# Kernel optimization log

Measured on AMD Instinct MI355X. Metric: run time of the kernel, lower is better.

## Reference

```python
import jax, jax.numpy as jnp
import numpy as np

N = 100000; E = 1600000; G = 2000; S = 40; MAXP = 50
IN = 64; F = 128; H = 4; HD = F // H; FFN = 8 * F
EPS = 1e-5; BN_EPS = 1e-5

def _ln(x, g, b):
    m = jnp.mean(x, -1, keepdims=True)
    v = jnp.mean((x - m) ** 2, -1, keepdims=True)
    return (x - m) * jax.lax.rsqrt(v + EPS) * g + b

def setup_inputs():
    key = jax.random.key(0)
    ks = jax.random.split(key, 16)
    def lin(k, i, o):
        kw, kb = jax.random.split(k)
        lim = 1.0 / np.sqrt(i)
        return (jax.random.uniform(kw, (i, o), jnp.float32, -lim, lim),
                jax.random.uniform(kb, (o,), jnp.float32, -lim, lim))
    W_gcn, b_gcn = lin(ks[1], IN, F)
    Wq, bq = lin(ks[2], F, F); Wk, bk = lin(ks[3], F, F)
    Wv, bv = lin(ks[4], F, F); Wo, bo = lin(ks[5], F, F)
    W1, b1 = lin(ks[6], F, FFN); W2, b2 = lin(ks[7], FFN, F)
    Wg, bg = lin(ks[8], 2 * F, F)
    ones = lambda: jnp.ones((F,), jnp.float32)
    zeros = lambda: jnp.zeros((F,), jnp.float32)
    return {
        'x': jax.random.normal(ks[0], (N, IN), jnp.float32),
        'edge_index': jax.random.randint(ks[9], (2, E), 0, N),
        'batch': jnp.repeat(jnp.arange(G), N // G),
        'set_batch': jnp.repeat(jnp.arange(S), G // S),
        'W_gcn': W_gcn, 'b_gcn': b_gcn,
        'bn_g': ones(), 'bn_b': zeros(),
        'lnpre_g': ones(), 'lnpre_b': zeros(),
        'Wq': Wq, 'bq': bq, 'Wk': Wk, 'bk': bk, 'Wv': Wv, 'bv': bv, 'Wo': Wo, 'bo': bo,
        'ln1_g': ones(), 'ln1_b': zeros(),
        'W1': W1, 'b1': b1, 'W2': W2, 'b2': b2,
        'ln2_g': ones(), 'ln2_b': zeros(),
        'Wg': Wg, 'bg': bg,
    }

def _forward(x, W_gcn, b_gcn, bn_g, bn_b, lnpre_g, lnpre_b, Wq, bq, Wk, bk, Wv, bv, Wo, bo, ln1_g, ln1_b, W1, b1, W2, b2, ln2_g, ln2_b, Wg, bg, edge_index, batch, set_batch):
    row, col = edge_index[0], edge_index[1]
    # GCNConv, improved=True -> self-loop weight 2.0 (PyG gcn_norm)
    xw = x @ W_gcn                                              # [N,F]
    deg = jax.ops.segment_sum(jnp.ones(E, xw.dtype), col, N) + 2.0
    dinv = jax.lax.rsqrt(deg)
    norm = dinv[row] * dinv[col]                                # [E]
    agg = jax.ops.segment_sum(xw[row] * norm[:, None], col, N)  # scatter-add to targets
    h = agg + (2.0 * dinv * dinv)[:, None] * xw + b_gcn
    # BatchNorm1d eval (running_mean=0, running_var=1) + ReLU; dropout is identity in eval
    h = jax.nn.relu(h * jax.lax.rsqrt(jnp.asarray(1.0 + BN_EPS, h.dtype)) * bn_g + bn_b)
    # global mean pool per graph
    cnt_g = jax.ops.segment_sum(jnp.ones(N, h.dtype), batch, G)
    z = jax.ops.segment_sum(h, batch, G) / cnt_g[:, None]       # [G,F]
    # to_dense_batch over sets (set_batch is sorted)
    cnt_s = jax.ops.segment_sum(jnp.ones(G, jnp.int32), set_batch, S)
    starts = jnp.cumsum(cnt_s) - cnt_s
    pos = jnp.arange(G) - starts[set_batch]                     # position within set
    zd = jnp.zeros((S, MAXP, F), z.dtype).at[set_batch, pos].set(z)
    mask = jnp.arange(MAXP)[None, :] < cnt_s[:, None]           # [S,MAXP]
    # pre-LN MHA with key_padding_mask
    zn = _ln(zd, lnpre_g, lnpre_b)
    q = (zn @ Wq + bq).reshape(S, MAXP, H, HD)
    k = (zn @ Wk + bk).reshape(S, MAXP, H, HD)
    v = (zn @ Wv + bv).reshape(S, MAXP, H, HD)
    scores = jnp.einsum('sqhd,skhd->shqk', q, k) / np.sqrt(HD)
    scores = jnp.where(mask[:, None, None, :], scores, -1e9)
    attn = jax.nn.softmax(scores, -1)
    o = jnp.einsum('shqk,skhd->sqhd', attn, v).reshape(S, MAXP, F) @ Wo + bo
    zd = _ln(zd + o, ln1_g, ln1_b)
    # FFN block (post-LN residual)
    f = jax.nn.relu(zd @ W1 + b1) @ W2 + b2
    zd = _ln(zd + f, ln2_g, ln2_b)
    # z_dense[mask] ordering == gather via (set_batch, pos); broadcast to nodes
    set_info = zd[set_batch, pos][batch]                        # [N,F]
    # gated fusion
    gate = jax.nn.sigmoid(jnp.concatenate([h, set_info], -1) @ Wg + bg)
    return gate * set_info + (1.0 - gate) * h

def reference(x, edge_index, batch, set_batch, W_gcn, b_gcn, bn_g, bn_b, lnpre_g, lnpre_b, Wq, bq, Wk, bk, Wv, bv, Wo, bo, ln1_g, ln1_b, W1, b1, W2, b2, ln2_g, ln2_b, Wg, bg):
    return _forward(x, W_gcn, b_gcn, bn_g, bn_b, lnpre_g, lnpre_b, Wq, bq, Wk, bk, Wv, bv, Wo, bo, ln1_g, ln1_b, W1, b1, W2, b2, ln2_g, ln2_b, Wg, bg, edge_index, batch, set_batch)
```

## Files before the change

kernel.cpp:

```cpp
#include <hip/hip_runtime.h>
#include <hip/hip_bf16.h>
#include <cstddef>

#define NN 100000
#define NE 1600000
#define NG 2000
#define NS 40
#define INF 64
#define F 128
#define FFN_DIM 1024
#define NB 782
#define BCAP 3072
#define SC_BLOCKS 512
#define SC_CHUNK 3125
#define NXB 782
#define NWB 72

using bf16 = __hip_bfloat16;
typedef __attribute__((ext_vector_type(8))) short short8;
typedef __attribute__((ext_vector_type(4))) float f32x4;
typedef __attribute__((ext_vector_type(2))) float f32x2;

__device__ __forceinline__ short f2bs(float f){
    union { bf16 b; short s; } u; u.b = __float2bfloat16(f); return u.s;
}
__device__ __forceinline__ unsigned int pk2(float a, float b){
    return (unsigned int)(unsigned short)f2bs(a) | ((unsigned int)(unsigned short)f2bs(b) << 16);
}

__global__ __launch_bounds__(256) void k_xws(const float* __restrict__ x, const float* __restrict__ W,
                                             const float* __restrict__ dinv, unsigned char* __restrict__ xws8,
                                             const float* __restrict__ Wq, const float* __restrict__ Wk,
                                             const float* __restrict__ Wv, const float* __restrict__ Wo,
                                             const float* __restrict__ W1, const float* __restrict__ W2,
                                             const float* __restrict__ Wg,
                                             unsigned short* __restrict__ Wqb, unsigned short* __restrict__ Wkb,
                                             unsigned short* __restrict__ Wvb, unsigned short* __restrict__ Wob,
                                             unsigned short* __restrict__ W1b, unsigned short* __restrict__ W2b,
                                             unsigned short* __restrict__ Wgb, unsigned short* __restrict__ Wgbotb){
    int t = threadIdx.x;
    if (blockIdx.x >= NXB){
        int wt = (blockIdx.x - NXB)*256 + t;
        const int ws = NWB*256;
        for (int i=wt; i<16384; i+=ws){
            int k = i>>7, n = i&127;
            Wqb[n*128+k]    = (unsigned short)f2bs(Wq[(size_t)k*F+n]);
            Wkb[n*128+k]    = (unsigned short)f2bs(Wk[(size_t)k*F+n]);
            Wvb[n*128+k]    = (unsigned short)f2bs(Wv[(size_t)k*F+n]);
            Wob[n*128+k]    = (unsigned short)f2bs(Wo[(size_t)k*F+n]);
            Wgb[n*128+k]    = (unsigned short)f2bs(Wg[(size_t)k*F+n]);
            Wgbotb[n*128+k] = (unsigned short)f2bs(Wg[(size_t)(F+k)*F+n]);
        }
        for (int i=wt; i<131072; i+=ws){
            int k = i>>10, n = i&1023;
            W1b[(size_t)n*128+k] = (unsigned short)f2bs(W1[(size_t)k*FFN_DIM+n]);
        }
        for (int i=wt; i<131072; i+=ws){
            int n = i>>10, k = i&1023;
            W2b[(size_t)n*1024+k] = (unsigned short)f2bs(W2[(size_t)k*F+n]);
        }
        return;
    }
    __shared__ short Xs[128*72];
    __shared__ short Ws[128*72];
    int rowBase = blockIdx.x * 128;
    #pragma unroll
    for (int i=0;i<32;i++){
        int id = i*256+t; int k = id>>7, n = id&127;
        Ws[n*72 + k] = f2bs(W[id]);
    }
    #pragma unroll
    for (int i=0;i<8;i++){
        int id = i*256+t;
        int r = id>>4; int k4 = (id&15)*4;
        int row = rowBase + r; if (row >= NN) row = NN-1;
        float4 v = *(const float4*)&x[(size_t)row*INF + k4];
        *(unsigned int*)&Xs[r*72 + k4]     = pk2(v.x, v.y);
        *(unsigned int*)&Xs[r*72 + k4 + 2] = pk2(v.z, v.w);
    }
    __syncthreads();
    int lane = t & 63, w = t >> 6;
    int lr = lane & 15, quad = lane >> 4;
    f32x4 acc[2][8];
    #pragma unroll
    for (int i=0;i<2;i++)
        #pragma unroll
        for (int j=0;j<8;j++) acc[i][j] = (f32x4){0.f,0.f,0.f,0.f};
    #pragma unroll
    for (int ks=0; ks<2; ++ks){
        int kb = ks*32 + quad*8;
        short8 b0 = *(const short8*)&Xs[((w  )*16 + lr)*72 + kb];
        short8 b1 = *(const short8*)&Xs[((w+4)*16 + lr)*72 + kb];
        #pragma unroll
        for (int mt=0; mt<8; ++mt){
            short8 a = *(const short8*)&Ws[(mt*16 + lr)*72 + kb];
            acc[0][mt] = __builtin_amdgcn_mfma_f32_16x16x32_bf16(a, b0, acc[0][mt], 0, 0, 0);
            acc[1][mt] = __builtin_amdgcn_mfma_f32_16x16x32_bf16(a, b1, acc[1][mt], 0, 0, 0);
        }
    }
    #pragma unroll
    for (int rt=0; rt<2; ++rt){
        int row = rowBase + (w + rt*4)*16 + lr;
        if (row < NN){
            float dv = dinv[row];
            #pragma unroll
            for (int mt=0; mt<8; ++mt){
                int p = __builtin_amdgcn_cvt_pk_fp8_f32(acc[rt][mt][0]*dv, acc[rt][mt][1]*dv, 0, false);
                p     = __builtin_amdgcn_cvt_pk_fp8_f32(acc[rt][mt][2]*dv, acc[rt][mt][3]*dv, p, true);
                *(int*)&xws8[(size_t)row*F + mt*16 + quad*4] = p;
            }
        }
    }
}

__global__ __launch_bounds__(1024) void k_scatter2(const int* __restrict__ ei, int* __restrict__ bcursor,
                                                   int* __restrict__ ebuf){
    __shared__ int lh[NB];
    __shared__ int lb[NB];
    int t = threadIdx.x;
    int base = blockIdx.x * SC_CHUNK;
    for (int b=t; b<NB; b+=1024) lh[b] = 0;
    __syncthreads();
    int rr[4], cc[4];
    #pragma unroll
    for (int q=0;q<4;q++){
        int i = t + q*1024;
        bool v = (i < SC_CHUNK);
        int idx = v ? (base + i) : base;
        rr[q] = ei[idx];
        cc[q] = ei[NE + idx];
        if (v) atomicAdd(&lh[cc[q]>>7], 1);
    }
    __syncthreads();
    for (int b=t; b<NB; b+=1024){
        int n = lh[b];
        lb[b] = n ? (b*BCAP + atomicAdd(&bcursor[b], n)) : 0;
        lh[b] = 0;
    }
    __syncthreads();
    #pragma unroll
    for (int q=0;q<4;q++){
        int i = t + q*1024;
        if (i < SC_CHUNK){
            int b = cc[q] >> 7;
            int rk = atomicAdd(&lh[b], 1);
            ebuf[lb[b] + rk] = (rr[q] << 7) | (cc[q] & 127);
        }
    }
}

__global__ __launch_bounds__(256) void k_sort(const int* __restrict__ ebuf, const int* __restrict__ bcursor,
                                              int* __restrict__ cnt, float* __restrict__ dinv,
                                              int* __restrict__ nstart, int* __restrict__ ebuf2){
    __shared__ int lh[128];
    __shared__ int s[128];
    __shared__ int lcur[128];
    __shared__ int sorted[BCAP];
    int t = threadIdx.x;
    int b = blockIdx.x;
    int e0 = b * BCAP;
    int nE = bcursor[b];
    if (t < 128) lh[t] = 0;
    __syncthreads();
    for (int i=t; i<nE; i+=256) atomicAdd(&lh[ebuf[e0+i] & 127], 1);
    __syncthreads();
    int c = (t < 128) ? lh[t] : 0;
    if (t < 128) s[t] = c;
    __syncthreads();
    #pragma unroll
    for (int off=1; off<128; off<<=1){
        int v = (t >= off && t < 128) ? s[t-off] : 0;
        __syncthreads();
        if (t < 128) s[t] += v;
        __syncthreads();
    }
    int node = b*128 + t;
    if (t < 128){
        int excl = s[t] - c;
        lcur[t] = excl;
        if (node < NN){
            nstart[node] = e0 + excl;
            cnt[node] = c;
            dinv[node] = rsqrtf((float)c + 2.0f);
        }
    }
    __syncthreads();
    for (int i=t; i<nE; i+=256){
        int v = ebuf[e0 + i];
        int nl = v & 127;
        int rk = atomicAdd(&lcur[nl], 1);
        sorted[rk] = (v >> 7) << 5;
    }
    __syncthreads();
    for (int i=t; i<nE; i+=256) ebuf2[e0 + i] = sorted[i];
}

__global__ __launch_bounds__(256) void k_aggpool(const unsigned char* __restrict__ xws8,
                                                 const int* __restrict__ nstart, const int* __restrict__ cnt,
                                                 const float* __restrict__ dinv, const float* __restrict__ b_gcn,
                                                 const float* __restrict__ bn_g, const float* __restrict__ bn_b,
                                                 const int* __restrict__ ebuf2,
                                                 const float* __restrict__ lnpre_g, const float* __restrict__ lnpre_b,
                                                 float* __restrict__ h, unsigned short* __restrict__ hb,
                                                 float* __restrict__ z, unsigned short* __restrict__ znb){
    __shared__ float zacc[4][128];
    int t = threadIdx.x;
    int lane = t & 63, w = t >> 6;
    int half = lane >> 5, lh = lane & 31;
    int g = blockIdx.x;
    const unsigned int* xw32 = (const unsigned int*)xws8;
    unsigned int* hb32 = (unsigned int*)hb;
    unsigned int* znb32 = (unsigned int*)znb;

    float4 bg4  = *(const float4*)&b_gcn[4*lh];
    float4 bng4 = *(const float4*)&bn_g[4*lh];
    float4 bnb4 = *(const float4*)&bn_b[4*lh];
    const float bns = rsqrtf(1.f + 1e-5f);

    float za0=0.f, za1=0.f, za2=0.f, za3=0.f;

    for (int i = w; i < 50; i += 4){
        int node = g*50 + i;
        int s0n = nstart[node]; int dg = cnt[node]; float dv = dinv[node];
        unsigned int us = xw32[node*32 + lh];
        float a0=0.f, a1=0.f, a2=0.f, a3=0.f;
        int j=0;
        for (; j+8<=dg; j+=8){
            int r0 = ebuf2[s0n+j+0+half];
            int r1 = ebuf2[s0n+j+2+half];
            int r2 = ebuf2[s0n+j+4+half];
            int r3 = ebuf2[s0n+j+6+half];
            unsigned int u0 = xw32[r0 + lh];
            unsigned int u1 = xw32[r1 + lh];
            unsigned int u2 = xw32[r2 + lh];
            unsigned int u3 = xw32[r3 + lh];
            f32x2 l0 = __builtin_amdgcn_cvt_pk_f32_fp8(u0, false);
            f32x2 h0 = __builtin_amdgcn_cvt_pk_f32_fp8(u0, true);
            f32x2 l1 = __builtin_amdgcn_cvt_pk_f32_fp8(u1, false);
            f32x2 h1 = __builtin_amdgcn_cvt_pk_f32_fp8(u1, true);
            f32x2 l2 = __builtin_amdgcn_cvt_pk_f32_fp8(u2, false);
            f32x2 h2 = __builtin_amdgcn_cvt_pk_f32_fp8(u2, true);
            f32x2 l3 = __builtin_amdgcn_cvt_pk_f32_fp8(u3, false);
            f32x2 h3 = __builtin_amdgcn_cvt_pk_f32_fp8(u3, true);
            a0 += (l0.x + l1.x) + (l2.x + l3.x);
            a1 += (l0.y + l1.y) + (l2.y + l3.y);
            a2 += (h0.x + h1.x) + (h2.x + h3.x);
            a3 += (h0.y + h1.y) + (h2.y + h3.y);
        }
        for (; j+2<=dg; j+=2){
            int r0 = ebuf2[s0n+j+half];
            unsigned int u0 = xw32[r0 + lh];
            f32x2 l0 = __builtin_amdgcn_cvt_pk_f32_fp8(u0, false);
            f32x2 h0 = __builtin_amdgcn_cvt_pk_f32_fp8(u0, true);
            a0 += l0.x; a1 += l0.y; a2 += h0.x; a3 += h0.y;
        }
        if (j < dg && half == 0){
            int r0 = ebuf2[s0n+j];
            unsigned int u0 = xw32[r0 + lh];
            f32x2 l0 = __builtin_amdgcn_cvt_pk_f32_fp8(u0, false);
            f32x2 h0 = __builtin_amdgcn_cvt_pk_f32_fp8(u0, true);
            a0 += l0.x; a1 += l0.y; a2 += h0.x; a3 += h0.y;
        }
        a0 += __shfl_xor(a0, 32);
        a1 += __shfl_xor(a1, 32);
        a2 += __shfl_xor(a2, 32);
        a3 += __shfl_xor(a3, 32);
        f32x2 fl = __builtin_amdgcn_cvt_pk_f32_fp8(us, false);
        f32x2 fh = __builtin_amdgcn_cvt_pk_f32_fp8(us, true);
        float p0 = dv*(a0 + 2.f*fl.x) + bg4.x;
        float p1 = dv*(a1 + 2.f*fl.y) + bg4.y;
        float p2 = dv*(a2 + 2.f*fh.x) + bg4.z;
        float p3 = dv*(a3 + 2.f*fh.y) + bg4.w;
        p0 = fmaxf(p0*bns*bng4.x + bnb4.x, 0.f);
        p1 = fmaxf(p1*bns*bng4.y + bnb4.y, 0.f);
        p2 = fmaxf(p2*bns*bng4.z + bnb4.z, 0.f);
        p3 = fmaxf(p3*bns*bng4.w + bnb4.w, 0.f);
        if (half == 0){
            *(float4*)&h[(size_t)node*F + 4*lh] = make_float4(p0,p1,p2,p3);
            *(uint2*)&hb32[(size_t)node*64 + 2*lh] = make_uint2(pk2(p0,p1), pk2(p2,p3));
        }
        za0 += p0; za1 += p1; za2 += p2; za3 += p3;
    }
    if (half == 0)
        *(float4*)&zacc[w][4*lh] = make_float4(za0, za1, za2, za3);
    __syncthreads();
    if (w == 0){
        float4 v0 = *(const float4*)&zacc[0][4*lh];
        float4 v1 = *(const float4*)&zacc[1][4*lh];
        float4 v2 = *(const float4*)&zacc[2][4*lh];
        float4 v3 = *(const float4*)&zacc[3][4*lh];
        float s0 = ((v0.x+v1.x)+(v2.x+v3.x)) / 50.0f;
        float s1 = ((v0.y+v1.y)+(v2.y+v3.y)) / 50.0f;
        float s2 = ((v0.z+v1.z)+(v2.z+v3.z)) / 50.0f;
        float s3 = ((v0.w+v1.w)+(v2.w+v3.w)) / 50.0f;
        if (half == 0)
            *(float4*)&z[(size_t)g*F + 4*lh] = make_float4(s0,s1,s2,s3);
        float s = (s0+s1)+(s2+s3);
        #pragma unroll
        for (int off=1; off<32; off<<=1) s += __shfl_xor(s, off);
        float m = s * (1.f/128.f);
        float d0=s0-m, d1=s1-m, d2=s2-m, d3=s3-m;
        float vv = (d0*d0+d1*d1)+(d2*d2+d3*d3);
        #pragma unroll
        for (int off=1; off<32; off<<=1) vv += __shfl_xor(vv, off);
        float rs = rsqrtf(vv*(1.f/128.f) + 1e-5f);
        float4 lg = *(const float4*)&lnpre_g[4*lh];
        float4 lb = *(const float4*)&lnpre_b[4*lh];
        if (half == 0){
            float o0 = d0*rs*lg.x+lb.x, o1 = d1*rs*lg.y+lb.y;
            float o2 = d2*rs*lg.z+lb.z, o3 = d3*rs*lg.w+lb.w;
            *(uint2*)&znb32[(size_t)g*64 + 2*lh] = make_uint2(pk2(o0,o1), pk2(o2,o3));
        }
    }
}

__global__ __launch_bounds__(256) void k_settf2(const unsigned short* __restrict__ znb,
                                                const float* __restrict__ z,
                                                const unsigned short* __restrict__ Wqb,
                                                const unsigned short* __restrict__ Wkb,
                                                const unsigned short* __restrict__ Wvb,
                                                const float* __restrict__ bq, const float* __restrict__ bk,
                                                const float* __restrict__ bv,
                                                const unsigned short* __restrict__ Wob, const float* __restrict__ bo,
                                                const float* __restrict__ ln1_g, const float* __restrict__ ln1_b,
                                                const unsigned short* __restrict__ W1b, const float* __restrict__ b1,
                                                const unsigned short* __restrict__ W2b, const float* __restrict__ b2,
                                                const float* __restrict__ ln2_g, const float* __restrict__ ln2_b,
                                                const unsigned short* __restrict__ Wgbotb, const float* __restrict__ bg,
                                                float* __restrict__ zd2, float* __restrict__ gsi){
    __shared__ __align__(16) char smem[138208];
    float* Sc   = (float*)smem;
    float* qs   = (float*)(smem + 41600);
    float* ks   = (float*)(smem + 68000);
    float* vs   = (float*)(smem + 94400);
    short* aob  = (short*)(smem + 120800);
    float* zd1f = (float*)(smem + 41600);
    short* zd1b = (short*)(smem + 68000);
    short* f1b  = (short*)(smem + 94400);
    short* zd2b = f1b;

    int t = threadIdx.x;
    int lane = t & 63, w = t >> 6;
    int lr = lane & 15, quad = lane >> 4;
    int s = blockIdx.x;
    const int r0 = s*50;

    {
        int rl = w*16 + lr; if (rl > 49) rl = 49;
        const unsigned short* arow = &znb[(size_t)(r0 + rl)*F];
        for (int zsel=0; zsel<3; ++zsel){
            const unsigned short* B = (zsel==0)?Wqb:(zsel==1)?Wkb:Wvb;
            const float* bp = (zsel==0)?bq:(zsel==1)?bk:bv;
            float* outp = (zsel==0)?qs:(zsel==1)?ks:vs;
            f32x4 acc[8];
            #pragma unroll
            for (int j=0;j<8;j++) acc[j] = (f32x4){0.f,0.f,0.f,0.f};
            #pragma unroll
            for (int ks4=0; ks4<4; ++ks4){
                int kb = ks4*32 + quad*8;
                short8 a = *(const short8*)&arow[kb];
                #pragma unroll
                for (int nt=0; nt<8; ++nt){
                    short8 b = *(const short8*)&B[(size_t)(nt*16 + lr)*128 + kb];
                    acc[nt] = __builtin_amdgcn_mfma_f32_16x16x32_bf16(a, b, acc[nt], 0, 0, 0);
                }
            }
            #pragma unroll
            for (int r=0; r<4; ++r){
                int row = w*16 + quad*4 + r;
                if (row < 50){
                    #pragma unroll
                    for (int nt=0; nt<8; ++nt){
                        int col = nt*16 + lr;
                        outp[row*132 + col] = acc[nt][r] + bp[col];
                    }
                }
            }
        }
    }
    __syncthreads();

    {
        int hh = w;
        float* ScH = Sc + hh*50*52;
        int qi = lane;
        if (qi < 50){
            float qreg[32];
            #pragma unroll
            for (int d=0; d<32; ++d) qreg[d] = qs[qi*132 + hh*32 + d];
            for (int ki=0; ki<50; ++ki){
                float acc=0.f;
                #pragma unroll
                for (int d=0; d<32; ++d) acc += qreg[d] * ks[ki*132 + hh*32 + d];
                ScH[qi*52 + ki] = acc * 0.17677669529663687f;
            }
            float m=-1e30f;
            for (int ki=0; ki<50; ++ki) m = fmaxf(m, ScH[qi*52+ki]);
            float sum=0.f;
            for (int ki=0; ki<50; ++ki){ float e=__expf(ScH[qi*52+ki]-m); ScH[qi*52+ki]=e; sum+=e; }
            float inv = 1.f/sum;
            float o[32];
            #pragma unroll
            for (int d=0; d<32; ++d) o[d] = 0.f;
            for (int ki=0; ki<50; ++ki){
                float sc = ScH[qi*52+ki] * inv;
                #pragma unroll
                for (int d=0; d<32; ++d) o[d] += sc * vs[ki*132 + hh*32 + d];
            }
            #pragma unroll
            for (int d=0; d<32; ++d) aob[qi*136 + hh*32 + d] = f2bs(o[d]);
        } else if (qi < 64){
            #pragma unroll
            for (int d=0; d<32; ++d) aob[qi*136 + hh*32 + d] = 0;
        }
    }
    __syncthreads();

    {
        f32x4 acc[8];
        #pragma unroll
        for (int j=0;j<8;j++) acc[j] = (f32x4){0.f,0.f,0.f,0.f};
        #pragma unroll
        for (int ks4=0; ks4<4; ++ks4){
            int kb = ks4*32 + quad*8;
            short8 a = *(const short8*)&aob[(w*16 + lr)*136 + kb];
            #pragma unroll
            for (int nt=0; nt<8; ++nt){
                short8 b = *(const short8*)&Wob[(size_t)(nt*16 + lr)*128 + kb];
                acc[nt] = __builtin_amdgcn_mfma_f32_16x16x32_bf16(a, b, acc[nt], 0, 0, 0);
            }
        }
        #pragma unroll
        for (int r=0; r<4; ++r){
            int row = w*16 + quad*4 + r;
            float v[8];
            if (row < 50){
                #pragma unroll
                for (int nt=0; nt<8; ++nt){
                    int col = nt*16 + lr;
                    v[nt] = acc[nt][r] + bo[col] + z[(size_t)(r0+row)*F + col];
                }
            } else {
                #pragma unroll
                for (int nt=0; nt<8; ++nt) v[nt] = 0.f;
            }
            float ssum = 0.f;
            #pragma unroll
            for (int nt=0; nt<8; ++nt) ssum += v[nt];
            #pragma unroll
            for (int off=1; off<16; off<<=1) ssum += __shfl_xor(ssum, off);
            float mean = ssum * (1.f/128.f);
            float var = 0.f;
            float d[8];
            #pragma unroll
            for (int nt=0; nt<8; ++nt){ d[nt] = v[nt]-mean; var += d[nt]*d[nt]; }
            #pragma unroll
            for (int off=1; off<16; off<<=1) var += __shfl_xor(var, off);
            float rsv = rsqrtf(var*(1.f/128.f) + 1e-5f);
            if (row < 50){
                #pragma unroll
                for (int nt=0; nt<8; ++nt){
                    int col = nt*16 + lr;
                    float o = d[nt]*rsv*ln1_g[col] + ln1_b[col];
                    zd1f[row*132 + col] = o;
                    zd1b[row*136 + col] = f2bs(o);
                }
            } else {
                #pragma unroll
                for (int nt=0; nt<8; ++nt) zd1b[row*136 + nt*16 + lr] = 0;
            }
        }
    }
    __syncthreads();

    f32x4 acc2[8];
    #pragma unroll
    for (int j=0;j<8;j++) acc2[j] = (f32x4){0.f,0.f,0.f,0.f};
    for (int c=0; c<8; ++c){
        f32x4 a1[8];
        #pragma unroll
        for (int j=0;j<8;j++) a1[j] = (f32x4){0.f,0.f,0.f,0.f};
        #pragma unroll
        for (int ks4=0; ks4<4; ++ks4){
            int kb = ks4*32 + quad*8;
            short8 a = *(const short8*)&zd1b[(w*16 + lr)*136 + kb];
            #pragma unroll
            for (int nt=0; nt<8; ++nt){
                short8 b = *(const short8*)&W1b[(size_t)(c*128 + nt*16 + lr)*128 + kb];
                a1[nt] = __builtin_amdgcn_mfma_f32_16x16x32_bf16(a, b, a1[nt], 0, 0, 0);
            }
        }
        #pragma unroll
        for (int r=0; r<4; ++r){
            int row = w*16 + quad*4 + r;
            #pragma unroll
            for (int nt=0; nt<8; ++nt){
                int col = nt*16 + lr;
                f1b[row*136 + col] = f2bs(fmaxf(a1[nt][r] + b1[c*128 + col], 0.f));
            }
        }
        __syncthreads();
        #pragma unroll
        for (int ks4=0; ks4<4; ++ks4){
            int kb = ks4*32 + quad*8;
            short8 a = *(const short8*)&f1b[(w*16 + lr)*136 + kb];
            #pragma unroll
            for (int nt=0; nt<8; ++nt){
                short8 b = *(const short8*)&W2b[(size_t)(nt*16 + lr)*1024 + c*128 + kb];
                acc2[nt] = __builtin_amdgcn_mfma_f32_16x16x32_bf16(a, b, acc2[nt], 0, 0, 0);
            }
        }
        __syncthreads();
    }

    {
        #pragma unroll
        for (int r=0; r<4; ++r){
            int row = w*16 + quad*4 + r;
            float v[8];
            if (row < 50){
                #pragma unroll
                for (int nt=0; nt<8; ++nt){
                    int col = nt*16 + lr;
                    v[nt] = acc2[nt][r] + b2[col] + zd1f[row*132 + col];
                }
            } else {
                #pragma unroll
                for (int nt=0; nt<8; ++nt) v[nt] = 0.f;
            }
            float ssum = 0.f;
            #pragma unroll
            for (int nt=0; nt<8; ++nt) ssum += v[nt];
            #pragma unroll
            for (int off=1; off<16; off<<=1) ssum += __shfl_xor(ssum, off);
            float mean = ssum * (1.f/128.f);
            float var = 0.f;
            float d[8];
            #pragma unroll
            for (int nt=0; nt<8; ++nt){ d[nt] = v[nt]-mean; var += d[nt]*d[nt]; }
            #pragma unroll
            for (int off=1; off<16; off<<=1) var += __shfl_xor(var, off);
            float rsv = rsqrtf(var*(1.f/128.f) + 1e-5f);
            if (row < 50){
                #pragma unroll
                for (int nt=0; nt<8; ++nt){
                    int col = nt*16 + lr;
                    float o = d[nt]*rsv*ln2_g[col] + ln2_b[col];
                    zd2[(size_t)(r0+row)*F + col] = o;
                    zd2b[row*136 + col] = f2bs(o);
                }
            } else {
                #pragma unroll
                for (int nt=0; nt<8; ++nt) zd2b[row*136 + nt*16 + lr] = 0;
            }
        }
        __syncthreads();
        f32x4 ag[8];
        #pragma unroll
        for (int j=0;j<8;j++) ag[j] = (f32x4){0.f,0.f,0.f,0.f};
        #pragma unroll
        for (int ks4=0; ks4<4; ++ks4){
            int kb = ks4*32 + quad*8;
            short8 a = *(const short8*)&zd2b[(w*16 + lr)*136 + kb];
            #pragma unroll
            for (int nt=0; nt<8; ++nt){
                short8 b = *(const short8*)&Wgbotb[(size_t)(nt*16 + lr)*128 + kb];
                ag[nt] = __builtin_amdgcn_mfma_f32_16x16x32_bf16(a, b, ag[nt], 0, 0, 0);
            }
        }
        #pragma unroll
        for (int r=0; r<4; ++r){
            int row = w*16 + quad*4 + r;
            if (row < 50){
                #pragma unroll
                for (int nt=0; nt<8; ++nt){
                    int col = nt*16 + lr;
                    gsi[(size_t)(r0+row)*F + col] = ag[nt][r] + bg[col];
                }
            }
        }
    }
}

__global__ __launch_bounds__(256) void k_gate_mfma(const float* __restrict__ h,
                                                   const unsigned short* __restrict__ hb,
                                                   const unsigned short* __restrict__ Wgb,
                                                   const float* __restrict__ gsi, const float* __restrict__ zd2,
                                                   float* __restrict__ out){
    int t = threadIdx.x;
    int lane = t & 63, w = t >> 6;
    int lr = lane & 15, quad = lane >> 4;
    int mrow0 = blockIdx.x*64 + w*16;
    f32x4 acc[8];
    #pragma unroll
    for (int j=0;j<8;j++) acc[j] = (f32x4){0.f,0.f,0.f,0.f};
    #pragma unroll
    for (int ks=0; ks<4; ++ks){
        int kb = ks*32 + quad*8;
        int row = mrow0 + lr;
        if (row >= NN) row = NN-1;
        short8 a = *(const short8*)&hb[(size_t)row*F + kb];
        #pragma unroll
        for (int nt=0; nt<8; ++nt){
            short8 b = *(const short8*)&Wgb[(size_t)(nt*16 + lr)*128 + kb];
            acc[nt] = __builtin_amdgcn_mfma_f32_16x16x32_bf16(a, b, acc[nt], 0, 0, 0);
        }
    }
    #pragma unroll
    for (int r=0; r<4; ++r){
        int row = mrow0 + quad*4 + r;
        if (row >= NN) continue;
        int g = row / 50;
        const float* gs = &gsi[(size_t)g*F];
        const float* zs = &zd2[(size_t)g*F];
        const float* hr = &h[(size_t)row*F];
        float* orow = &out[(size_t)row*F];
        #pragma unroll
        for (int nt=0; nt<8; ++nt){
            int col = nt*16 + lr;
            float L = acc[nt][r] + gs[col];
            float gate = 1.f/(1.f + __expf(-L));
            orow[col] = gate*zs[col] + (1.f-gate)*hr[col];
        }
    }
}

extern "C" void kernel_launch(void* const* d_in, const int* in_sizes, int n_in,
                              void* d_out, int out_size, void* d_ws, size_t ws_size,
                              hipStream_t stream) {
    const float* x      = (const float*)d_in[0];
    const int*   ei     = (const int*)d_in[1];
    const float* W_gcn  = (const float*)d_in[4];
    const float* b_gcn  = (const float*)d_in[5];
    const float* bn_g   = (const float*)d_in[6];
    const float* bn_b   = (const float*)d_in[7];
    const float* lnpre_g= (const float*)d_in[8];
    const float* lnpre_b= (const float*)d_in[9];
    const float* Wq     = (const float*)d_in[10];
    const float* bq     = (const float*)d_in[11];
    const float* Wk     = (const float*)d_in[12];
    const float* bk     = (const float*)d_in[13];
    const float* Wv     = (const float*)d_in[14];
    const float* bv     = (const float*)d_in[15];
    const float* Wo     = (const float*)d_in[16];
    const float* bo     = (const float*)d_in[17];
    const float* ln1_g  = (const float*)d_in[18];
    const float* ln1_b  = (const float*)d_in[19];
    const float* W1     = (const float*)d_in[20];
    const float* b1     = (const float*)d_in[21];
    const float* W2     = (const float*)d_in[22];
    const float* b2     = (const float*)d_in[23];
    const float* ln2_g  = (const float*)d_in[24];
    const float* ln2_b  = (const float*)d_in[25];
    const float* Wg     = (const float*)d_in[26];
    const float* bg     = (const float*)d_in[27];
    float* out = (float*)d_out;
    char* ws = (char*)d_ws;

    size_t o = 0;
    unsigned char* xws8 = (unsigned char*)(ws + o); o += (size_t)NN*F;
    float* h     = (float*)(ws + o); o += (size_t)NN*F*4;
    unsigned short* hb = (unsigned short*)(ws + o); o += (size_t)NN*F*2;
    int*   cnt   = (int*)(ws + o);   o += (size_t)NN*4;
    int*   nstart= (int*)(ws + o);   o += (size_t)NN*4;
    int*   ebuf  = (int*)(ws + o);   o += (size_t)NB*BCAP*4;
    int*   ebuf2 = (int*)(ws + o);   o += (size_t)NB*BCAP*4;
    float* dinv  = (float*)(ws + o); o += (size_t)NN*4;
    int*   bcursor=(int*)(ws + o);   o += 1024*4;
    unsigned short* Wgb    = (unsigned short*)(ws + o); o += 16384*2;
    unsigned short* Wqb    = (unsigned short*)(ws + o); o += 16384*2;
    unsigned short* Wkb    = (unsigned short*)(ws + o); o += 16384*2;
    unsigned short* Wvb    = (unsigned short*)(ws + o); o += 16384*2;
    unsigned short* Wob    = (unsigned short*)(ws + o); o += 16384*2;
    unsigned short* Wgbotb = (unsigned short*)(ws + o); o += 16384*2;
    unsigned short* W1b = (unsigned short*)(ws + o); o += (size_t)131072*2;
    unsigned short* W2b = (unsigned short*)(ws + o); o += (size_t)131072*2;
    float* z     = (float*)(ws + o); o += (size_t)NG*F*4;
    unsigned short* znb = (unsigned short*)(ws + o); o += (size_t)NG*F*2;
    float* zd2   = (float*)(ws + o); o += (size_t)NG*F*4;
    float* gsi   = (float*)(ws + o); o += (size_t)NG*F*4;

    hipMemsetAsync(bcursor, 0, (size_t)NB*4, stream);
    k_scatter2<<<SC_BLOCKS, 1024, 0, stream>>>(ei, bcursor, ebuf);
    k_sort<<<NB, 256, 0, stream>>>(ebuf, bcursor, cnt, dinv, nstart, ebuf2);
    k_xws<<<NXB + NWB, 256, 0, stream>>>(x, W_gcn, dinv, xws8,
                                         Wq, Wk, Wv, Wo, W1, W2, Wg,
                                         Wqb, Wkb, Wvb, Wob, W1b, W2b, Wgb, Wgbotb);
    k_aggpool<<<NG, 256, 0, stream>>>(xws8, nstart, cnt, dinv, b_gcn, bn_g, bn_b, ebuf2,
                                      lnpre_g, lnpre_b, h, hb, z, znb);

    k_settf2<<<NS, 256, 0, stream>>>(znb, z, Wqb, Wkb, Wvb, bq, bk, bv,
                                     Wob, bo, ln1_g, ln1_b, W1b, b1, W2b, b2,
                                     ln2_g, ln2_b, Wgbotb, bg, zd2, gsi);

    k_gate_mfma<<<(NN+63)/64, 256, 0, stream>>>(h, hb, Wgb, gsi, zd2, out);
}
```

Baseline: 373.4 us.

## Split set transformer into QKV-in-pool, per-head attention, and row-tiled post kernels

Replaces the single set-transformer kernel, which ran on only 40 blocks, with three stages. The Q/K/V projections are folded into the pooling kernel as per-graph fp32 matvecs, attention runs in a separate kernel with one block per set and head (160 blocks), and the Wo/LN/FFN/LN/gate projection runs in a 16-row-tiled MFMA kernel over 125 blocks. The aim is to remove the low-parallelism serial tail. In exchange it adds two kernel launches and global round trips for q/k/v/attention output, and the QKV projection now uses fp32 scalar math with uncached weight reads.

```diff
diff --git a/kernel.cpp b/kernel.cpp
--- a/kernel.cpp
+++ b/kernel.cpp
@@ -30,23 +30,17 @@
 
 __global__ __launch_bounds__(256) void k_xws(const float* __restrict__ x, const float* __restrict__ W,
                                              const float* __restrict__ dinv, unsigned char* __restrict__ xws8,
-                                             const float* __restrict__ Wq, const float* __restrict__ Wk,
-                                             const float* __restrict__ Wv, const float* __restrict__ Wo,
-                                             const float* __restrict__ W1, const float* __restrict__ W2,
-                                             const float* __restrict__ Wg,
-                                             unsigned short* __restrict__ Wqb, unsigned short* __restrict__ Wkb,
-                                             unsigned short* __restrict__ Wvb, unsigned short* __restrict__ Wob,
-                                             unsigned short* __restrict__ W1b, unsigned short* __restrict__ W2b,
-                                             unsigned short* __restrict__ Wgb, unsigned short* __restrict__ Wgbotb){
+                                             const float* __restrict__ Wo, const float* __restrict__ W1,
+                                             const float* __restrict__ W2, const float* __restrict__ Wg,
+                                             unsigned short* __restrict__ Wob, unsigned short* __restrict__ W1b,
+                                             unsigned short* __restrict__ W2b, unsigned short* __restrict__ Wgb,
+                                             unsigned short* __restrict__ Wgbotb){
     int t = threadIdx.x;
     if (blockIdx.x >= NXB){
         int wt = (blockIdx.x - NXB)*256 + t;
         const int ws = NWB*256;
         for (int i=wt; i<16384; i+=ws){
             int k = i>>7, n = i&127;
-            Wqb[n*128+k]    = (unsigned short)f2bs(Wq[(size_t)k*F+n]);
-            Wkb[n*128+k]    = (unsigned short)f2bs(Wk[(size_t)k*F+n]);
-            Wvb[n*128+k]    = (unsigned short)f2bs(Wv[(size_t)k*F+n]);
             Wob[n*128+k]    = (unsigned short)f2bs(Wo[(size_t)k*F+n]);
             Wgb[n*128+k]    = (unsigned short)f2bs(Wg[(size_t)k*F+n]);
             Wgbotb[n*128+k] = (unsigned short)f2bs(Wg[(size_t)(F+k)*F+n]);
@@ -201,8 +195,13 @@
                                                  const float* __restrict__ bn_g, const float* __restrict__ bn_b,
                                                  const int* __restrict__ ebuf2,
                                                  const float* __restrict__ lnpre_g, const float* __restrict__ lnpre_b,
+                                                 const float* __restrict__ Wq, const float* __restrict__ bq,
+                                                 const float* __restrict__ Wk, const float* __restrict__ bk,
+                                                 const float* __restrict__ Wv, const float* __restrict__ bv,
                                                  float* __restrict__ h, unsigned short* __restrict__ hb,
-                                                 float* __restrict__ z, unsigned short* __restrict__ znb){
+                                                 float* __restrict__ z,
+                                                 float* __restrict__ qb, float* __restrict__ kb2,
+                                                 float* __restrict__ vb){
     __shared__ float zacc[4][128];
     int t = threadIdx.x;
     int lane = t & 63, w = t >> 6;
@@ -210,7 +209,6 @@
     int g = blockIdx.x;
     const unsigned int* xw32 = (const unsigned int*)xws8;
     unsigned int* hb32 = (unsigned int*)hb;
-    unsigned int* znb32 = (unsigned int*)znb;
 
     float4 bg4  = *(const float4*)&b_gcn[4*lh];
     float4 bng4 = *(const float4*)&bn_g[4*lh];
@@ -307,276 +305,235 @@
         float4 lg = *(const float4*)&lnpre_g[4*lh];
         float4 lb = *(const float4*)&lnpre_b[4*lh];
         if (half == 0){
-            float o0 = d0*rs*lg.x+lb.x, o1 = d1*rs*lg.y+lb.y;
-            float o2 = d2*rs*lg.z+lb.z, o3 = d3*rs*lg.w+lb.w;
-            *(uint2*)&znb32[(size_t)g*64 + 2*lh] = make_uint2(pk2(o0,o1), pk2(o2,o3));
-        }
-    }
-}
-
-__global__ __launch_bounds__(256) void k_settf2(const unsigned short* __restrict__ znb,
-                                                const float* __restrict__ z,
-                                                const unsigned short* __restrict__ Wqb,
-                                                const unsigned short* __restrict__ Wkb,
-                                                const unsigned short* __restrict__ Wvb,
-                                                const float* __restrict__ bq, const float* __restrict__ bk,
-                                                const float* __restrict__ bv,
-                                                const unsigned short* __restrict__ Wob, const float* __restrict__ bo,
-                                                const float* __restrict__ ln1_g, const float* __restrict__ ln1_b,
-                                                const unsigned short* __restrict__ W1b, const float* __restrict__ b1,
-                                                const unsigned short* __restrict__ W2b, const float* __restrict__ b2,
-                                                const float* __restrict__ ln2_g, const float* __restrict__ ln2_b,
-                                                const unsigned short* __restrict__ Wgbotb, const float* __restrict__ bg,
-                                                float* __restrict__ zd2, float* __restrict__ gsi){
-    __shared__ __align__(16) char smem[138208];
-    float* Sc   = (float*)smem;
-    float* qs   = (float*)(smem + 41600);
-    float* ks   = (float*)(smem + 68000);
-    float* vs   = (float*)(smem + 94400);
-    short* aob  = (short*)(smem + 120800);
-    float* zd1f = (float*)(smem + 41600);
-    short* zd1b = (short*)(smem + 68000);
-    short* f1b  = (short*)(smem + 94400);
-    short* zd2b = f1b;
-
+            zacc[0][4*lh]   = d0*rs*lg.x+lb.x;
+            zacc[0][4*lh+1] = d1*rs*lg.y+lb.y;
+            zacc[0][4*lh+2] = d2*rs*lg.z+lb.z;
+            zacc[0][4*lh+3] = d3*rs*lg.w+lb.w;
+        }
+    }
+    __syncthreads();
+    for (int idx = t; idx < 384; idx += 256){
+        int sel = idx >> 7, col = idx & 127;
+        const float* Wp = (sel==0) ? Wq : (sel==1) ? Wk : Wv;
+        const float* bi = (sel==0) ? bq : (sel==1) ? bk : bv;
+        float* C = (sel==0) ? qb : (sel==1) ? kb2 : vb;
+        float acc = bi[col];
+        #pragma unroll 4
+        for (int k=0; k<128; ++k) acc += zacc[0][k] * Wp[(size_t)k*F + col];
+        C[(size_t)g*F + col] = acc;
+    }
+}
+
+__global__ __launch_bounds__(256) void k_attn(const float* __restrict__ q, const float* __restrict__ k,
+                                              const float* __restrict__ v, unsigned short* __restrict__ aob){
+    __shared__ float Qs[1600], Ks[1600], Vs[1600], Sc[2500];
+    int t = threadIdx.x;
+    int s = blockIdx.x >> 2; int hh = blockIdx.x & 3;
+    for (int idx=t; idx<1600; idx+=256){
+        int i = idx>>5, d = idx&31;
+        size_t gi = (size_t)(s*50+i)*F + hh*32 + d;
+        Qs[idx]=q[gi]; Ks[idx]=k[gi]; Vs[idx]=v[gi];
+    }
+    __syncthreads();
+    for (int idx=t; idx<2500; idx+=256){
+        int qi = idx/50, ki = idx%50;
+        float acc=0.f;
+        #pragma unroll 8
+        for (int d=0;d<32;d++) acc += Qs[qi*32+d]*Ks[ki*32+d];
+        Sc[idx] = acc * 0.17677669529663687f;
+    }
+    __syncthreads();
+    if (t < 50){
+        float m=-1e30f;
+        for (int j=0;j<50;j++) m = fmaxf(m, Sc[t*50+j]);
+        float sum=0.f;
+        for (int j=0;j<50;j++){ float e=__expf(Sc[t*50+j]-m); Sc[t*50+j]=e; sum+=e; }
+        float inv = 1.f/sum;
+        for (int j=0;j<50;j++) Sc[t*50+j] *= inv;
+    }
+    __syncthreads();
+    for (int idx=t; idx<1600; idx+=256){
+        int qi = idx>>5, d = idx&31;
+        float acc=0.f;
+        #pragma unroll 10
+        for (int ki=0;ki<50;ki++) acc += Sc[qi*50+ki]*Vs[ki*32+d];
+        aob[(size_t)(s*50+qi)*F + hh*32 + d] = (unsigned short)f2bs(acc);
+    }
+}
+
+__global__ __launch_bounds__(256) void k_post(const unsigned short* __restrict__ aob,
+                                              const float* __restrict__ z,
+                                              const unsigned short* __restrict__ Wob, const float* __restrict__ bo,
+                                              const float* __restrict__ ln1_g, const float* __restrict__ ln1_b,
+                                              const unsigned short* __restrict__ W1b, const float* __restrict__ b1,
+                                              const unsigned short* __restrict__ W2b, const float* __restrict__ b2,
+                                              const float* __restrict__ ln2_g, const float* __restrict__ ln2_b,
+                                              const unsigned short* __restrict__ Wgbotb, const float* __restrict__ bg,
+                                              float* __restrict__ zd2, float* __restrict__ gsi){
+    __shared__ float zd1f[16*132];
+    __shared__ short zd1b[16*136];
+    __shared__ short f1b[16*1040];
+    __shared__ short zd2b[16*136];
     int t = threadIdx.x;
     int lane = t & 63, w = t >> 6;
     int lr = lane & 15, quad = lane >> 4;
-    int s = blockIdx.x;
-    const int r0 = s*50;
+    int gr0 = blockIdx.x * 16;
 
     {
-        int rl = w*16 + lr; if (rl > 49) rl = 49;
-        const unsigned short* arow = &znb[(size_t)(r0 + rl)*F];
-        for (int zsel=0; zsel<3; ++zsel){
-            const unsigned short* B = (zsel==0)?Wqb:(zsel==1)?Wkb:Wvb;
-            const float* bp = (zsel==0)?bq:(zsel==1)?bk:bv;
-            float* outp = (zsel==0)?qs:(zsel==1)?ks:vs;
-            f32x4 acc[8];
+        f32x4 accA[2];
+        accA[0] = (f32x4){0.f,0.f,0.f,0.f};
+        accA[1] = (f32x4){0.f,0.f,0.f,0.f};
+        #pragma unroll
+        for (int ks4=0; ks4<4; ++ks4){
+            int kb = ks4*32 + quad*8;
+            short8 a = *(const short8*)&aob[(size_t)(gr0 + lr)*F + kb];
             #pragma unroll
-            for (int j=0;j<8;j++) acc[j] = (f32x4){0.f,0.f,0.f,0.f};
+            for (int j=0;j<2;j++){
+                int nt = 2*w + j;
+                short8 b = *(const short8*)&Wob[(size_t)(nt*16 + lr)*128 + kb];
+                accA[j] = __builtin_amdgcn_mfma_f32_16x16x32_bf16(a, b, accA[j], 0, 0, 0);
+            }
+        }
+        #pragma unroll
+        for (int j=0;j<2;j++){
+            int nt = 2*w + j;
+            #pragma unroll
+            for (int r=0;r<4;r++){
+                int row = quad*4 + r;
+                int col = nt*16 + lr;
+                zd1f[row*132 + col] = accA[j][r] + bo[col] + z[(size_t)(gr0+row)*F + col];
+            }
+        }
+    }
+    __syncthreads();
+    {
+        int tr = t >> 4, l16 = t & 15;
+        float v[8];
+        #pragma unroll
+        for (int i=0;i<8;i++) v[i] = zd1f[tr*132 + l16*8 + i];
+        float s = 0.f;
+        #pragma unroll
+        for (int i=0;i<8;i++) s += v[i];
+        #pragma unroll
+        for (int off=1; off<16; off<<=1) s += __shfl_xor(s, off);
+        float mean = s * (1.f/128.f);
+        float var = 0.f;
+        float d[8];
+        #pragma unroll
+        for (int i=0;i<8;i++){ d[i] = v[i]-mean; var += d[i]*d[i]; }
+        #pragma unroll
+        for (int off=1; off<16; off<<=1) var += __shfl_xor(var, off);
+        float rsv = rsqrtf(var*(1.f/128.f) + 1e-5f);
+        #pragma unroll
+        for (int i=0;i<8;i++){
+            int c = l16*8 + i;
+            float o = d[i]*rsv*ln1_g[c] + ln1_b[c];
+            zd1f[tr*132 + c] = o;
+            zd1b[tr*136 + c] = f2bs(o);
+        }
+    }
+    __syncthreads();
+
+    {
+        short8 a[4];
+        #pragma unroll
+        for (int ks4=0; ks4<4; ++ks4){
+            int kb = ks4*32 + quad*8;
+            a[ks4] = *(const short8*)&zd1b[lr*136 + kb];
+        }
+        for (int nt2=0; nt2<16; ++nt2){
+            int coln = w*256 + nt2*16 + lr;
+            f32x4 acc = (f32x4){0.f,0.f,0.f,0.f};
             #pragma unroll
             for (int ks4=0; ks4<4; ++ks4){
                 int kb = ks4*32 + quad*8;
-                short8 a = *(const short8*)&arow[kb];
-                #pragma unroll
-                for (int nt=0; nt<8; ++nt){
-                    short8 b = *(const short8*)&B[(size_t)(nt*16 + lr)*128 + kb];
-                    acc[nt] = __builtin_amdgcn_mfma_f32_16x16x32_bf16(a, b, acc[nt], 0, 0, 0);
-                }
+                short8 b = *(const short8*)&W1b[(size_t)coln*128 + kb];
+                acc = __builtin_amdgcn_mfma_f32_16x16x32_bf16(a[ks4], b, acc, 0, 0, 0);
             }
             #pragma unroll
-            for (int r=0; r<4; ++r){
-                int row = w*16 + quad*4 + r;
-                if (row < 50){
-                    #pragma unroll
-                    for (int nt=0; nt<8; ++nt){
-                        int col = nt*16 + lr;
-                        outp[row*132 + col] = acc[nt][r] + bp[col];
-                    }
-                }
+            for (int r=0;r<4;r++){
+                int row = quad*4 + r;
+                int col = w*256 + nt2*16 + lr;
+                f1b[row*1040 + col] = f2bs(fmaxf(acc[r] + b1[col], 0.f));
             }
         }
     }
     __syncthreads();
 
+    f32x4 accC[2];
+    accC[0] = (f32x4){0.f,0.f,0.f,0.f};
+    accC[1] = (f32x4){0.f,0.f,0.f,0.f};
+    for (int ks4=0; ks4<32; ++ks4){
+        int kb = ks4*32 + quad*8;
+        short8 a = *(const short8*)&f1b[lr*1040 + kb];
+        #pragma unroll
+        for (int j=0;j<2;j++){
+            int nt = 2*w + j;
+            short8 b = *(const short8*)&W2b[(size_t)(nt*16 + lr)*1024 + kb];
+            accC[j] = __builtin_amdgcn_mfma_f32_16x16x32_bf16(a, b, accC[j], 0, 0, 0);
+        }
+    }
+    #pragma unroll
+    for (int j=0;j<2;j++){
+        int nt = 2*w + j;
+        #pragma unroll
+        for (int r=0;r<4;r++){
+            int row = quad*4 + r;
+            int col = nt*16 + lr;
+            zd1f[row*132 + col] = accC[j][r] + b2[col] + zd1f[row*132 + col];
+        }
+    }
+    __syncthreads();
     {
-        int hh = w;
-        float* ScH = Sc + hh*50*52;
-        int qi = lane;
-        if (qi < 50){
-            float qreg[32];
-            #pragma unroll
-            for (int d=0; d<32; ++d) qreg[d] = qs[qi*132 + hh*32 + d];
-            for (int ki=0; ki<50; ++ki){
-                float acc=0.f;
-                #pragma unroll
-                for (int d=0; d<32; ++d) acc += qreg[d] * ks[ki*132 + hh*32 + d];
-                ScH[qi*52 + ki] = acc * 0.17677669529663687f;
-            }
-            float m=-1e30f;
-            for (int ki=0; ki<50; ++ki) m = fmaxf(m, ScH[qi*52+ki]);
-            float sum=0.f;
-            for (int ki=0; ki<50; ++ki){ float e=__expf(ScH[qi*52+ki]-m); ScH[qi*52+ki]=e; sum+=e; }
-            float inv = 1.f/sum;
-            float o[32];
-            #pragma unroll
-            for (int d=0; d<32; ++d) o[d] = 0.f;
-            for (int ki=0; ki<50; ++ki){
-                float sc = ScH[qi*52+ki] * inv;
-                #pragma unroll
-                for (int d=0; d<32; ++d) o[d] += sc * vs[ki*132 + hh*32 + d];
-            }
-            #pragma unroll
-            for (int d=0; d<32; ++d) aob[qi*136 + hh*32 + d] = f2bs(o[d]);
-        } else if (qi < 64){
-            #pragma unroll
-            for (int d=0; d<32; ++d) aob[qi*136 + hh*32 + d] = 0;
-        }
-    }
-    __syncthreads();
-
+        int tr = t >> 4, l16 = t & 15;
+        float v[8];
+        #pragma unroll
+        for (int i=0;i<8;i++) v[i] = zd1f[tr*132 + l16*8 + i];
+        float s = 0.f;
+        #pragma unroll
+        for (int i=0;i<8;i++) s += v[i];
+        #pragma unroll
+        for (int off=1; off<16; off<<=1) s += __shfl_xor(s, off);
+        float mean = s * (1.f/128.f);
+        float var = 0.f;
+        float d[8];
+        #pragma unroll
+        for (int i=0;i<8;i++){ d[i] = v[i]-mean; var += d[i]*d[i]; }
+        #pragma unroll
+        for (int off=1; off<16; off<<=1) var += __shfl_xor(var, off);
+        float rsv = rsqrtf(var*(1.f/128.f) + 1e-5f);
+        #pragma unroll
+        for (int i=0;i<8;i++){
+            int c = l16*8 + i;
+            float o = d[i]*rsv*ln2_g[c] + ln2_b[c];
+            zd2[(size_t)(gr0+tr)*F + c] = o;
+            zd2b[tr*136 + c] = f2bs(o);
+        }
+    }
+    __syncthreads();
     {
-        f32x4 acc[8];
-        #pragma unroll
-        for (int j=0;j<8;j++) acc[j] = (f32x4){0.f,0.f,0.f,0.f};
+        f32x4 accG[2];
+        accG[0] = (f32x4){0.f,0.f,0.f,0.f};
+        accG[1] = (f32x4){0.f,0.f,0.f,0.f};
         #pragma unroll
         for (int ks4=0; ks4<4; ++ks4){
             int kb = ks4*32 + quad*8;
-            short8 a = *(const short8*)&aob[(w*16 + lr)*136 + kb];
+            short8 a = *(const short8*)&zd2b[lr*136 + kb];
             #pragma unroll
-            for (int nt=0; nt<8; ++nt){
-                short8 b = *(const short8*)&Wob[(size_t)(nt*16 + lr)*128 + kb];
-                acc[nt] = __builtin_amdgcn_mfma_f32_16x16x32_bf16(a, b, acc[nt], 0, 0, 0);
+            for (int j=0;j<2;j++){
+                int nt = 2*w + j;
+                short8 b = *(const short8*)&Wgbotb[(size_t)(nt*16 + lr)*128 + kb];
+                accG[j] = __builtin_amdgcn_mfma_f32_16x16x32_bf16(a, b, accG[j], 0, 0, 0);
             }
         }
         #pragma unroll
-        for (int r=0; r<4; ++r){
-            int row = w*16 + quad*4 + r;
-            float v[8];
-            if (row < 50){
-                #pragma unroll
-                for (int nt=0; nt<8; ++nt){
-                    int col = nt*16 + lr;
-                    v[nt] = acc[nt][r] + bo[col] + z[(size_t)(r0+row)*F + col];
-                }
-            } else {
-                #pragma unroll
-                for (int nt=0; nt<8; ++nt) v[nt] = 0.f;
-            }
-            float ssum = 0.f;
+        for (int j=0;j<2;j++){
+            int nt = 2*w + j;
             #pragma unroll
-            for (int nt=0; nt<8; ++nt) ssum += v[nt];
-            #pragma unroll
-            for (int off=1; off<16; off<<=1) ssum += __shfl_xor(ssum, off);
-            float mean = ssum * (1.f/128.f);
-            float var = 0.f;
-            float d[8];
-            #pragma unroll
-            for (int nt=0; nt<8; ++nt){ d[nt] = v[nt]-mean; var += d[nt]*d[nt]; }
-            #pragma unroll
-            for (int off=1; off<16; off<<=1) var += __shfl_xor(var, off);
-            float rsv = rsqrtf(var*(1.f/128.f) + 1e-5f);
-            if (row < 50){
-                #pragma unroll
-                for (int nt=0; nt<8; ++nt){
-                    int col = nt*16 + lr;
-                    float o = d[nt]*rsv*ln1_g[col] + ln1_b[col];
-                    zd1f[row*132 + col] = o;
-                    zd1b[row*136 + col] = f2bs(o);
-                }
-            } else {
-                #pragma unroll
-                for (int nt=0; nt<8; ++nt) zd1b[row*136 + nt*16 + lr] = 0;
-            }
-        }
-    }
-    __syncthreads();
-
-    f32x4 acc2[8];
-    #pragma unroll
-    for (int j=0;j<8;j++) acc2[j] = (f32x4){0.f,0.f,0.f,0.f};
-    for (int c=0; c<8; ++c){
-        f32x4 a1[8];
-        #pragma unroll
-        for (int j=0;j<8;j++) a1[j] = (f32x4){0.f,0.f,0.f,0.f};
-        #pragma unroll
-        for (int ks4=0; ks4<4; ++ks4){
-            int kb = ks4*32 + quad*8;
-            short8 a = *(const short8*)&zd1b[(w*16 + lr)*136 + kb];
-            #pragma unroll
-            for (int nt=0; nt<8; ++nt){
-                short8 b = *(const short8*)&W1b[(size_t)(c*128 + nt*16 + lr)*128 + kb];
-                a1[nt] = __builtin_amdgcn_mfma_f32_16x16x32_bf16(a, b, a1[nt], 0, 0, 0);
-            }
-        }
-        #pragma unroll
-        for (int r=0; r<4; ++r){
-            int row = w*16 + quad*4 + r;
-            #pragma unroll
-            for (int nt=0; nt<8; ++nt){
+            for (int r=0;r<4;r++){
+                int row = quad*4 + r;
                 int col = nt*16 + lr;
-                f1b[row*136 + col] = f2bs(fmaxf(a1[nt][r] + b1[c*128 + col], 0.f));
-            }
-        }
-        __syncthreads();
-        #pragma unroll
-        for (int ks4=0; ks4<4; ++ks4){
-            int kb = ks4*32 + quad*8;
-            short8 a = *(const short8*)&f1b[(w*16 + lr)*136 + kb];
-            #pragma unroll
-            for (int nt=0; nt<8; ++nt){
-                short8 b = *(const short8*)&W2b[(size_t)(nt*16 + lr)*1024 + c*128 + kb];
-                acc2[nt] = __builtin_amdgcn_mfma_f32_16x16x32_bf16(a, b, acc2[nt], 0, 0, 0);
-            }
-        }
-        __syncthreads();
-    }
-
-    {
-        #pragma unroll
-        for (int r=0; r<4; ++r){
-            int row = w*16 + quad*4 + r;
-            float v[8];
-            if (row < 50){
-                #pragma unroll
-                for (int nt=0; nt<8; ++nt){
-                    int col = nt*16 + lr;
-                    v[nt] = acc2[nt][r] + b2[col] + zd1f[row*132 + col];
-                }
-            } else {
-                #pragma unroll
-                for (int nt=0; nt<8; ++nt) v[nt] = 0.f;
-            }
-            float ssum = 0.f;
-            #pragma unroll
-            for (int nt=0; nt<8; ++nt) ssum += v[nt];
-            #pragma unroll
-            for (int off=1; off<16; off<<=1) ssum += __shfl_xor(ssum, off);
-            float mean = ssum * (1.f/128.f);
-            float var = 0.f;
-            float d[8];
-            #pragma unroll
-            for (int nt=0; nt<8; ++nt){ d[nt] = v[nt]-mean; var += d[nt]*d[nt]; }
-            #pragma unroll
-            for (int off=1; off<16; off<<=1) var += __shfl_xor(var, off);
-            float rsv = rsqrtf(var*(1.f/128.f) + 1e-5f);
-            if (row < 50){
-                #pragma unroll
-                for (int nt=0; nt<8; ++nt){
-                    int col = nt*16 + lr;
-                    float o = d[nt]*rsv*ln2_g[col] + ln2_b[col];
-                    zd2[(size_t)(r0+row)*F + col] = o;
-                    zd2b[row*136 + col] = f2bs(o);
-                }
-            } else {
-                #pragma unroll
-                for (int nt=0; nt<8; ++nt) zd2b[row*136 + nt*16 + lr] = 0;
-            }
-        }
-        __syncthreads();
-        f32x4 ag[8];
-        #pragma unroll
-        for (int j=0;j<8;j++) ag[j] = (f32x4){0.f,0.f,0.f,0.f};
-        #pragma unroll
-        for (int ks4=0; ks4<4; ++ks4){
-            int kb = ks4*32 + quad*8;
-            short8 a = *(const short8*)&zd2b[(w*16 + lr)*136 + kb];
-            #pragma unroll
-            for (int nt=0; nt<8; ++nt){
-                short8 b = *(const short8*)&Wgbotb[(size_t)(nt*16 + lr)*128 + kb];
-                ag[nt] = __builtin_amdgcn_mfma_f32_16x16x32_bf16(a, b, ag[nt], 0, 0, 0);
-            }
-        }
-        #pragma unroll
-        for (int r=0; r<4; ++r){
-            int row = w*16 + quad*4 + r;
-            if (row < 50){
-                #pragma unroll
-                for (int nt=0; nt<8; ++nt){
-                    int col = nt*16 + lr;
-                    gsi[(size_t)(r0+row)*F + col] = ag[nt][r] + bg[col];
-                }
+                gsi[(size_t)(gr0+row)*F + col] = accG[j][r] + bg[col];
             }
         }
     }
@@ -668,15 +625,15 @@
     float* dinv  = (float*)(ws + o); o += (size_t)NN*4;
     int*   bcursor=(int*)(ws + o);   o += 1024*4;
     unsigned short* Wgb    = (unsigned short*)(ws + o); o += 16384*2;
-    unsigned short* Wqb    = (unsigned short*)(ws + o); o += 16384*2;
-    unsigned short* Wkb    = (unsigned short*)(ws + o); o += 16384*2;
-    unsigned short* Wvb    = (unsigned short*)(ws + o); o += 16384*2;
     unsigned short* Wob    = (unsigned short*)(ws + o); o += 16384*2;
     unsigned short* Wgbotb = (unsigned short*)(ws + o); o += 16384*2;
     unsigned short* W1b = (unsigned short*)(ws + o); o += (size_t)131072*2;
     unsigned short* W2b = (unsigned short*)(ws + o); o += (size_t)131072*2;
     float* z     = (float*)(ws + o); o += (size_t)NG*F*4;
-    unsigned short* znb = (unsigned short*)(ws + o); o += (size_t)NG*F*2;
+    float* qb    = (float*)(ws + o); o += (size_t)NG*F*4;
+    float* kb2   = (float*)(ws + o); o += (size_t)NG*F*4;
+    float* vb    = (float*)(ws + o); o += (size_t)NG*F*4;
+    unsigned short* aob = (unsigned short*)(ws + o); o += (size_t)NG*F*2;
     float* zd2   = (float*)(ws + o); o += (size_t)NG*F*4;
     float* gsi   = (float*)(ws + o); o += (size_t)NG*F*4;
 
@@ -684,14 +641,15 @@
     k_scatter2<<<SC_BLOCKS, 1024, 0, stream>>>(ei, bcursor, ebuf);
     k_sort<<<NB, 256, 0, stream>>>(ebuf, bcursor, cnt, dinv, nstart, ebuf2);
     k_xws<<<NXB + NWB, 256, 0, stream>>>(x, W_gcn, dinv, xws8,
-                                         Wq, Wk, Wv, Wo, W1, W2, Wg,
-                                         Wqb, Wkb, Wvb, Wob, W1b, W2b, Wgb, Wgbotb);
+                                         Wo, W1, W2, Wg,
+                                         Wob, W1b, W2b, Wgb, Wgbotb);
     k_aggpool<<<NG, 256, 0, stream>>>(xws8, nstart, cnt, dinv, b_gcn, bn_g, bn_b, ebuf2,
-                                      lnpre_g, lnpre_b, h, hb, z, znb);
-
-    k_settf2<<<NS, 256, 0, stream>>>(znb, z, Wqb, Wkb, Wvb, bq, bk, bv,
-                                     Wob, bo, ln1_g, ln1_b, W1b, b1, W2b, b2,
-                                     ln2_g, ln2_b, Wgbotb, bg, zd2, gsi);
+                                      lnpre_g, lnpre_b, Wq, bq, Wk, bk, Wv, bv,
+                                      h, hb, z, qb, kb2, vb);
+
+    k_attn<<<NS*4, 256, 0, stream>>>(qb, kb2, vb, aob);
+    k_post<<<NG/16, 256, 0, stream>>>(aob, z, Wob, bo, ln1_g, ln1_b, W1b, b1,
+                                      W2b, b2, ln2_g, ln2_b, Wgbotb, bg, zd2, gsi);
 
     k_gate_mfma<<<(NN+63)/64, 256, 0, stream>>>(h, hb, Wgb, gsi, zd2, out);
 }
```

New measurement: 312.9 us. 1.19x faster.
